# Optimization experiments

Hardware: AMD Instinct MI355X
Metric: run time of the kernel (lower is better)

## Reference

```python
import jax, jax.numpy as jnp
import numpy as np

NUM_HEADS = 12

def rel_indices(N):
    # [N, N, 3] = (dx, dy, dist^2) between patches on an img x img grid
    img = int(N ** 0.5)
    ind = jnp.arange(img)[None, :] - jnp.arange(img)[:, None]      # [img, img]
    indx = jnp.tile(ind, (img, img))                               # [N, N]
    indy = jnp.repeat(jnp.repeat(ind, img, axis=0), img, axis=1)   # [N, N]
    indd = indx ** 2 + indy ** 2
    return jnp.stack([indx, indy, indd], axis=-1).astype(jnp.float32)

def setup_inputs() -> dict:
    key = jax.random.key(0)
    ks = jax.random.split(key, 8)
    B, N, C, H = 16, 576, 768, NUM_HEADS
    std = 0.02  # trunc_normal init scale in the original
    return {
        "x": jax.random.normal(ks[0], (B, N, C), jnp.float32),
        "w_qk": jax.random.normal(ks[1], (C, 2 * C), jnp.float32) * std,
        "w_v": jax.random.normal(ks[2], (C, C), jnp.float32) * std,
        "w_proj": jax.random.normal(ks[3], (C, C), jnp.float32) * std,
        "b_proj": jnp.zeros((C,), jnp.float32),
        "w_pos": jax.random.normal(ks[4], (3, H), jnp.float32) * std,
        "b_pos": jnp.zeros((H,), jnp.float32),
        "gating": jnp.ones((H,), jnp.float32),
    }

def reference(x, w_qk, w_v, w_proj, b_proj, w_pos, b_pos, gating):
    B, N, C = x.shape
    H = NUM_HEADS
    Dh = C // H
    scale = Dh ** -0.5

    # q, k: [B, H, N, Dh]
    qk = (x @ w_qk).reshape(B, N, 2, H, Dh)
    q = jnp.transpose(qk[:, :, 0], (0, 2, 1, 3))
    k = jnp.transpose(qk[:, :, 1], (0, 2, 1, 3))

    # content scores, softmax over keys
    patch_score = jax.nn.softmax(
        jnp.einsum("bhnd,bhmd->bhnm", q, k) * scale, axis=-1)

    # positional scores: rel_indices [N,N,3] -> [H,N,N], softmax over keys
    rel = rel_indices(N)
    pos_logits = jnp.einsum("nmk,kh->hnm", rel, w_pos) + b_pos[:, None, None]
    pos_score = jax.nn.softmax(pos_logits, axis=-1)  # [H, N, N]

    # sigmoid gating + renormalization
    g = jax.nn.sigmoid(gating)[None, :, None, None]
    attn = (1.0 - g) * patch_score + g * pos_score[None]
    attn = attn / jnp.sum(attn, axis=-1, keepdims=True)

    # v: [B, H, N, Dh]
    v = jnp.transpose((x @ w_v).reshape(B, N, H, Dh), (0, 2, 1, 3))

    out = jnp.einsum("bhnm,bhmd->bnhd", attn, v).reshape(B, N, C)
    out = out @ w_proj + b_proj
    return (out, attn, v)
```

## Files before the change

kernel.cpp:

```cpp
#include <hip/hip_runtime.h>
#include <hip/hip_bf16.h>

typedef __bf16 bf16;
typedef __attribute__((ext_vector_type(4))) __bf16 bf16x4;
typedef __attribute__((ext_vector_type(8))) __bf16 bf16x8;
typedef __attribute__((ext_vector_type(4))) float floatx4;

#define BB 16
#define NN 576
#define CC 768
#define HH 12
#define DH 64

__global__ void k_convert(const float* __restrict__ in, bf16* __restrict__ out, int n4){
  int i = blockIdx.x*blockDim.x + threadIdx.x;
  if (i < n4){
    float4 f = ((const float4*)in)[i];
    bf16x4 o;
    o[0]=(bf16)f.x; o[1]=(bf16)f.y; o[2]=(bf16)f.z; o[3]=(bf16)f.w;
    ((bf16x4*)out)[i] = o;
  }
}

__global__ void k_transpose(const float* __restrict__ src, bf16* __restrict__ dst, int R, int Cc){
  __shared__ float tile[32][33];
  int c0 = blockIdx.x*32, r0 = blockIdx.y*32;
  int tx = threadIdx.x & 31, ty = threadIdx.x >> 5;
  #pragma unroll
  for (int i=0;i<4;i++)
    tile[ty + i*8][tx] = src[(size_t)(r0 + ty + i*8)*Cc + c0 + tx];
  __syncthreads();
  #pragma unroll
  for (int i=0;i<4;i++)
    dst[(size_t)(c0 + ty + i*8)*R + r0 + tx] = (bf16)tile[tx][ty + i*8];
}

__global__ __launch_bounds__(256) void k_pos(const float* __restrict__ w_pos, float* __restrict__ pos){
  int t = threadIdx.x, wv = t>>6, lane = t&63;
  int rowid = blockIdx.x*4 + wv;
  int h = rowid / NN, n = rowid % NN;
  float w0 = w_pos[h], w1 = w_pos[HH + h], w2 = w_pos[2*HH + h];
  int nx = n % 24, ny = n / 24;
  float e[9]; float mx = -1e30f;
  #pragma unroll
  for (int j=0;j<9;j++){
    int m = lane + 64*j;
    float dx = (float)(m % 24 - nx);
    float dy = (float)(m / 24 - ny);
    float l = dx*w0 + dy*w1 + (dx*dx + dy*dy)*w2;
    e[j] = l; mx = fmaxf(mx, l);
  }
  #pragma unroll
  for (int s=1;s<64;s<<=1) mx = fmaxf(mx, __shfl_xor(mx, s, 64));
  float sum = 0.f;
  #pragma unroll
  for (int j=0;j<9;j++){ e[j] = __expf(e[j]-mx); sum += e[j]; }
  #pragma unroll
  for (int s=1;s<64;s<<=1) sum += __shfl_xor(sum, s, 64);
  float inv = 1.f/sum;
  float* dst = pos + (size_t)rowid*NN;
  #pragma unroll
  for (int j=0;j<9;j++) dst[lane + 64*j] = e[j]*inv;
}

__device__ __forceinline__ void gemm_main_bf16(
    const bf16* __restrict__ A, const bf16* __restrict__ Bt,
    int lda, int ldb, int K, int rowBase, int colBase,
    bf16 (*As)[40], bf16 (*Bs)[40], floatx4* acc)
{
  int t = threadIdx.x;
  int sr = t >> 2, scg = (t & 3) * 8;
  int wv = t >> 6, m16 = t & 15, q = (t & 63) >> 4;
  for (int k0 = 0; k0 < K; k0 += 32){
    *(bf16x8*)&As[sr][scg] = *(const bf16x8*)&A[(size_t)(rowBase + sr)*lda + k0 + scg];
    *(bf16x8*)&Bs[sr][scg] = *(const bf16x8*)&Bt[(size_t)(colBase + sr)*ldb + k0 + scg];
    __syncthreads();
    bf16x8 bfr = *(const bf16x8*)&Bs[wv*16 + m16][q*8];
    #pragma unroll
    for (int rt=0; rt<4; rt++){
      bf16x8 afr = *(const bf16x8*)&As[rt*16 + m16][q*8];
      acc[rt] = __builtin_amdgcn_mfma_f32_16x16x32_bf16(afr, bfr, acc[rt], 0, 0, 0);
    }
    __syncthreads();
  }
}

__device__ __forceinline__ void gemm_main_f32A(
    const float* __restrict__ A, const bf16* __restrict__ Bt,
    int lda, int ldb, int K, int rowBase, int colBase,
    bf16 (*As)[40], bf16 (*Bs)[40], floatx4* acc)
{
  int t = threadIdx.x;
  int sr = t >> 2, scg = (t & 3) * 8;
  int wv = t >> 6, m16 = t & 15, q = (t & 63) >> 4;
  for (int k0 = 0; k0 < K; k0 += 32){
    float4 f0 = *(const float4*)&A[(size_t)(rowBase + sr)*lda + k0 + scg];
    float4 f1 = *(const float4*)&A[(size_t)(rowBase + sr)*lda + k0 + scg + 4];
    bf16x8 av;
    av[0]=(bf16)f0.x; av[1]=(bf16)f0.y; av[2]=(bf16)f0.z; av[3]=(bf16)f0.w;
    av[4]=(bf16)f1.x; av[5]=(bf16)f1.y; av[6]=(bf16)f1.z; av[7]=(bf16)f1.w;
    *(bf16x8*)&As[sr][scg] = av;
    *(bf16x8*)&Bs[sr][scg] = *(const bf16x8*)&Bt[(size_t)(colBase + sr)*ldb + k0 + scg];
    __syncthreads();
    bf16x8 bfr = *(const bf16x8*)&Bs[wv*16 + m16][q*8];
    #pragma unroll
    for (int rt=0; rt<4; rt++){
      bf16x8 afr = *(const bf16x8*)&As[rt*16 + m16][q*8];
      acc[rt] = __builtin_amdgcn_mfma_f32_16x16x32_bf16(afr, bfr, acc[rt], 0, 0, 0);
    }
    __syncthreads();
  }
}

__global__ __launch_bounds__(256) void k_gemm1(
    const bf16* __restrict__ x_bf, const bf16* __restrict__ wcatT,
    bf16* __restrict__ q_bf, bf16* __restrict__ k_bf,
    bf16* __restrict__ vt_bf, float* __restrict__ v_out)
{
  __shared__ bf16 As[64][40];
  __shared__ bf16 Bs[64][40];
  int cb = blockIdx.x % 36, rb = blockIdx.x / 36;
  int rowBase = rb*64, colBase = cb*64;
  floatx4 acc[4] = {{0.f,0.f,0.f,0.f},{0.f,0.f,0.f,0.f},{0.f,0.f,0.f,0.f},{0.f,0.f,0.f,0.f}};
  gemm_main_bf16(x_bf, wcatT, CC, CC, CC, rowBase, colBase, As, Bs, acc);
  int wv = threadIdx.x >> 6, m16 = threadIdx.x & 15, q = (threadIdx.x & 63) >> 4;
  int col = colBase + wv*16 + m16;
  #pragma unroll
  for (int rt=0; rt<4; rt++){
    #pragma unroll
    for (int i=0;i<4;i++){
      int row = rowBase + rt*16 + q*4 + i;
      float val = acc[rt][i];
      int b = row / NN, n = row % NN;
      if (col < 2*CC){
        int s = col / CC, rem = col % CC;
        int h = rem >> 6, d = rem & 63;
        bf16* dst = s ? k_bf : q_bf;
        dst[(((b*HH + h)*NN + n) << 6) + d] = (bf16)val;
      } else {
        int rem = col - 2*CC;
        int h = rem >> 6, d = rem & 63;
        v_out[(((b*HH + h)*NN + n) << 6) + d] = val;
        vt_bf[((b*HH + h)*DH + d)*NN + n] = (bf16)val;
      }
    }
  }
}

__global__ __launch_bounds__(256) void k_attn(
    const bf16* __restrict__ q_bf, const bf16* __restrict__ k_bf,
    const float* __restrict__ pos, const float* __restrict__ gating,
    float* __restrict__ attn_out)
{
  __shared__ bf16 Qs[16][72];
  __shared__ bf16 Ks[64][72];
  __shared__ float S[16][592];
  int qt = blockIdx.x % 36, bh = blockIdx.x / 36;
  int h = bh % HH;
  int n0 = qt*16;
  int t = threadIdx.x;
  int wv = t>>6, m16 = t&15, q = (t&63)>>4;
  const bf16* Qg = q_bf + ((size_t)bh*NN + n0)*DH;
  const bf16* Kg = k_bf + (size_t)bh*NN*DH;
  { int r = t >> 4, c4 = (t & 15)*4;
    *(bf16x4*)&Qs[r][c4] = *(const bf16x4*)&Qg[r*DH + c4]; }
  for (int kt=0; kt<9; kt++){
    __syncthreads();
    { int r = t>>2, cg = (t&3)*16;
      *(bf16x8*)&Ks[r][cg]   = *(const bf16x8*)&Kg[(kt*64 + r)*DH + cg];
      *(bf16x8*)&Ks[r][cg+8] = *(const bf16x8*)&Kg[(kt*64 + r)*DH + cg + 8]; }
    __syncthreads();
    floatx4 acc = {0.f,0.f,0.f,0.f};
    #pragma unroll
    for (int ks=0; ks<2; ks++){
      bf16x8 afr = *(const bf16x8*)&Qs[m16][ks*32 + q*8];
      bf16x8 bfr = *(const bf16x8*)&Ks[wv*16 + m16][ks*32 + q*8];
      acc = __builtin_amdgcn_mfma_f32_16x16x32_bf16(afr, bfr, acc, 0, 0, 0);
    }
    #pragma unroll
    for (int i=0;i<4;i++)
      S[q*4 + i][kt*64 + wv*16 + m16] = acc[i] * 0.125f;
  }
  __syncthreads();
  int row = t >> 4, sub = t & 15;
  int n = n0 + row;
  float vals[36];
  float mx = -1e30f;
  #pragma unroll
  for (int j=0;j<36;j++){ float xv = S[row][sub + 16*j]; vals[j]=xv; mx = fmaxf(mx,xv); }
  #pragma unroll
  for (int s=1;s<16;s<<=1) mx = fmaxf(mx, __shfl_xor(mx, s, 64));
  float ps = 0.f;
  #pragma unroll
  for (int j=0;j<36;j++){ vals[j] = __expf(vals[j]-mx); ps += vals[j]; }
  #pragma unroll
  for (int s=1;s<16;s<<=1) ps += __shfl_xor(ps, s, 64);
  float g = 1.f/(1.f + __expf(-gating[h]));
  float ig = (1.f - g)/ps;
  const float* posrow = pos + ((size_t)h*NN + n)*NN;
  float bs = 0.f;
  #pragma unroll
  for (int j=0;j<36;j++){ float a = ig*vals[j] + g*posrow[sub + 16*j]; vals[j]=a; bs += a; }
  #pragma unroll
  for (int s=1;s<16;s<<=1) bs += __shfl_xor(bs, s, 64);
  float inv = 1.f/bs;
  float* arow = attn_out + ((size_t)bh*NN + n)*NN;
  #pragma unroll
  for (int j=0;j<36;j++) arow[sub + 16*j] = vals[j]*inv;
}

__global__ __launch_bounds__(256) void k_pv(
    const float* __restrict__ attn, const bf16* __restrict__ vt_bf,
    bf16* __restrict__ out1_bf)
{
  __shared__ bf16 As[64][40];
  __shared__ bf16 Bs[64][40];
  int rb = blockIdx.x % 9, bh = blockIdx.x / 9;
  int b = bh / HH, h = bh % HH;
  const float* Ap = attn + (size_t)bh*NN*NN;
  const bf16* Bp = vt_bf + (size_t)bh*DH*NN;
  floatx4 acc[4] = {{0.f,0.f,0.f,0.f},{0.f,0.f,0.f,0.f},{0.f,0.f,0.f,0.f},{0.f,0.f,0.f,0.f}};
  gemm_main_f32A(Ap, Bp, NN, NN, NN, rb*64, 0, As, Bs, acc);
  int wv = threadIdx.x >> 6, m16 = threadIdx.x & 15, q = (threadIdx.x & 63) >> 4;
  int d = wv*16 + m16;
  #pragma unroll
  for (int rt=0; rt<4; rt++){
    #pragma unroll
    for (int i=0;i<4;i++){
      int n = rb*64 + rt*16 + q*4 + i;
      out1_bf[(size_t)(b*NN + n)*CC + h*DH + d] = (bf16)acc[rt][i];
    }
  }
}

__global__ __launch_bounds__(256) void k_proj(
    const bf16* __restrict__ out1_bf, const bf16* __restrict__ wprojT,
    const float* __restrict__ b_proj, float* __restrict__ out)
{
  __shared__ bf16 As[64][40];
  __shared__ bf16 Bs[64][40];
  int cb = blockIdx.x % 12, rb = blockIdx.x / 12;
  floatx4 acc[4] = {{0.f,0.f,0.f,0.f},{0.f,0.f,0.f,0.f},{0.f,0.f,0.f,0.f},{0.f,0.f,0.f,0.f}};
  gemm_main_bf16(out1_bf, wprojT, CC, CC, CC, rb*64, cb*64, As, Bs, acc);
  int wv = threadIdx.x >> 6, m16 = threadIdx.x & 15, q = (threadIdx.x & 63) >> 4;
  int col = cb*64 + wv*16 + m16;
  float bias = b_proj[col];
  #pragma unroll
  for (int rt=0; rt<4; rt++){
    #pragma unroll
    for (int i=0;i<4;i++){
      int row = rb*64 + rt*16 + q*4 + i;
      out[(size_t)row*CC + col] = acc[rt][i] + bias;
    }
  }
}

extern "C" void kernel_launch(void* const* d_in, const int* in_sizes, int n_in,
                              void* d_out, int out_size, void* d_ws, size_t ws_size,
                              hipStream_t stream)
{
  (void)in_sizes; (void)n_in; (void)out_size; (void)ws_size;
  const float* x      = (const float*)d_in[0];
  const float* w_qk   = (const float*)d_in[1];
  const float* w_v    = (const float*)d_in[2];
  const float* w_proj = (const float*)d_in[3];
  const float* b_proj = (const float*)d_in[4];
  const float* w_pos  = (const float*)d_in[5];
  const float* gating = (const float*)d_in[7];

  float* out_ptr  = (float*)d_out;
  float* attn_ptr = out_ptr + (size_t)BB*NN*CC;
  float* v_ptr    = attn_ptr + (size_t)BB*HH*NN*NN;

  char* w = (char*)d_ws;
  bf16* x_bf    = (bf16*)(w);
  bf16* wcatT   = (bf16*)(w + 14155776);
  bf16* wprojT  = (bf16*)(w + 17694720);
  bf16* q_bf    = (bf16*)(w + 18874368);
  bf16* k_bf    = (bf16*)(w + 33030144);
  bf16* vt_bf   = (bf16*)(w + 47185920);
  float* pos    = (float*)(w + 61341696);
  bf16* out1_bf = x_bf;

  k_convert<<<6912, 256, 0, stream>>>(x, x_bf, (BB*NN*CC)/4);
  k_transpose<<<dim3(48,24), 256, 0, stream>>>(w_qk, wcatT, CC, 2*CC);
  k_transpose<<<dim3(24,24), 256, 0, stream>>>(w_v, wcatT + (size_t)2*CC*CC, CC, CC);
  k_transpose<<<dim3(24,24), 256, 0, stream>>>(w_proj, wprojT, CC, CC);
  k_pos<<<(HH*NN)/4, 256, 0, stream>>>(w_pos, pos);
  k_gemm1<<<144*36, 256, 0, stream>>>(x_bf, wcatT, q_bf, k_bf, vt_bf, v_ptr);
  k_attn<<<192*36, 256, 0, stream>>>(q_bf, k_bf, pos, gating, attn_ptr);
  k_pv<<<192*9, 256, 0, stream>>>(attn_ptr, vt_bf, out1_bf);
  k_proj<<<144*12, 256, 0, stream>>>(out1_bf, wprojT, b_proj, out_ptr);
}
```

Before: 593.5 us.

## Fuse PV into attention kernel and use 128x128 LDS-direct GEMM tiles

Fuses the P@V product into the attention kernel. Normalized probabilities are written as bf16 into the reused score buffer in shared memory and multiplied against V^T there, so the 127MB fp32 attention matrix is no longer re-read from global memory. The QKV and projection GEMMs move to 128x128 tiles with four waves each computing 64x64 through 16 MFMAs per k-step. Their tiles are loaded with global_load_lds direct-to-LDS transfers. This raises per-block register use and needs the swizzled LDS layout to be consistent, while the fused kernel adds a barrier and an extra shared-memory pass.

```diff
diff --git a/kernel.cpp b/kernel.cpp
--- a/kernel.cpp
+++ b/kernel.cpp
@@ -11,6 +11,10 @@
 #define CC 768
 #define HH 12
 #define DH 64
+
+#define GLOAD_LDS16(gp, lp) __builtin_amdgcn_global_load_lds( \
+    (const __attribute__((address_space(1))) unsigned int*)(const void*)(gp), \
+    (__attribute__((address_space(3))) unsigned int*)(void*)(lp), 16, 0, 0)
 
 __global__ void k_convert(const float* __restrict__ in, bf16* __restrict__ out, int n4){
   int i = blockIdx.x*blockDim.x + threadIdx.x;
@@ -63,51 +67,32 @@
   for (int j=0;j<9;j++) dst[lane + 64*j] = e[j]*inv;
 }
 
-__device__ __forceinline__ void gemm_main_bf16(
-    const bf16* __restrict__ A, const bf16* __restrict__ Bt,
-    int lda, int ldb, int K, int rowBase, int colBase,
-    bf16 (*As)[40], bf16 (*Bs)[40], floatx4* acc)
-{
-  int t = threadIdx.x;
-  int sr = t >> 2, scg = (t & 3) * 8;
-  int wv = t >> 6, m16 = t & 15, q = (t & 63) >> 4;
+__device__ __forceinline__ void gemm128_main(
+    const bf16* __restrict__ A, const bf16* __restrict__ B,
+    int lda, int ldb, int K, bf16* As, bf16* Bs, floatx4 (*acc)[4])
+{
+  int t = threadIdx.x;
+  int w = t>>6, m16 = t&15, q = (t&63)>>4;
+  int wr = (w>>1)*64, wc = (w&1)*64;
+  int sr = t>>2, kg = (t&3)*8;
+  bf16* ldsA = As + w*512;
+  bf16* ldsB = Bs + w*512;
   for (int k0 = 0; k0 < K; k0 += 32){
-    *(bf16x8*)&As[sr][scg] = *(const bf16x8*)&A[(size_t)(rowBase + sr)*lda + k0 + scg];
-    *(bf16x8*)&Bs[sr][scg] = *(const bf16x8*)&Bt[(size_t)(colBase + sr)*ldb + k0 + scg];
-    __syncthreads();
-    bf16x8 bfr = *(const bf16x8*)&Bs[wv*16 + m16][q*8];
-    #pragma unroll
-    for (int rt=0; rt<4; rt++){
-      bf16x8 afr = *(const bf16x8*)&As[rt*16 + m16][q*8];
-      acc[rt] = __builtin_amdgcn_mfma_f32_16x16x32_bf16(afr, bfr, acc[rt], 0, 0, 0);
-    }
-    __syncthreads();
-  }
-}
-
-__device__ __forceinline__ void gemm_main_f32A(
-    const float* __restrict__ A, const bf16* __restrict__ Bt,
-    int lda, int ldb, int K, int rowBase, int colBase,
-    bf16 (*As)[40], bf16 (*Bs)[40], floatx4* acc)
-{
-  int t = threadIdx.x;
-  int sr = t >> 2, scg = (t & 3) * 8;
-  int wv = t >> 6, m16 = t & 15, q = (t & 63) >> 4;
-  for (int k0 = 0; k0 < K; k0 += 32){
-    float4 f0 = *(const float4*)&A[(size_t)(rowBase + sr)*lda + k0 + scg];
-    float4 f1 = *(const float4*)&A[(size_t)(rowBase + sr)*lda + k0 + scg + 4];
-    bf16x8 av;
-    av[0]=(bf16)f0.x; av[1]=(bf16)f0.y; av[2]=(bf16)f0.z; av[3]=(bf16)f0.w;
-    av[4]=(bf16)f1.x; av[5]=(bf16)f1.y; av[6]=(bf16)f1.z; av[7]=(bf16)f1.w;
-    *(bf16x8*)&As[sr][scg] = av;
-    *(bf16x8*)&Bs[sr][scg] = *(const bf16x8*)&Bt[(size_t)(colBase + sr)*ldb + k0 + scg];
-    __syncthreads();
-    bf16x8 bfr = *(const bf16x8*)&Bs[wv*16 + m16][q*8];
-    #pragma unroll
-    for (int rt=0; rt<4; rt++){
-      bf16x8 afr = *(const bf16x8*)&As[rt*16 + m16][q*8];
-      acc[rt] = __builtin_amdgcn_mfma_f32_16x16x32_bf16(afr, bfr, acc[rt], 0, 0, 0);
-    }
+    GLOAD_LDS16(A + (size_t)sr*lda      + k0 + kg, ldsA);
+    GLOAD_LDS16(A + (size_t)(sr+64)*lda + k0 + kg, ldsA + 2048);
+    GLOAD_LDS16(B + (size_t)sr*ldb      + k0 + kg, ldsB);
+    GLOAD_LDS16(B + (size_t)(sr+64)*ldb + k0 + kg, ldsB + 2048);
+    __syncthreads();
+    bf16x8 af[4], bfv[4];
+    #pragma unroll
+    for (int rt=0;rt<4;rt++) af[rt]  = *(const bf16x8*)&As[(wr + rt*16 + m16)*32 + q*8];
+    #pragma unroll
+    for (int ct=0;ct<4;ct++) bfv[ct] = *(const bf16x8*)&Bs[(wc + ct*16 + m16)*32 + q*8];
+    #pragma unroll
+    for (int rt=0;rt<4;rt++)
+      #pragma unroll
+      for (int ct=0;ct<4;ct++)
+        acc[rt][ct] = __builtin_amdgcn_mfma_f32_16x16x32_bf16(af[rt], bfv[ct], acc[rt][ct], 0, 0, 0);
     __syncthreads();
   }
 }
@@ -117,46 +102,57 @@
     bf16* __restrict__ q_bf, bf16* __restrict__ k_bf,
     bf16* __restrict__ vt_bf, float* __restrict__ v_out)
 {
-  __shared__ bf16 As[64][40];
-  __shared__ bf16 Bs[64][40];
-  int cb = blockIdx.x % 36, rb = blockIdx.x / 36;
-  int rowBase = rb*64, colBase = cb*64;
-  floatx4 acc[4] = {{0.f,0.f,0.f,0.f},{0.f,0.f,0.f,0.f},{0.f,0.f,0.f,0.f},{0.f,0.f,0.f,0.f}};
-  gemm_main_bf16(x_bf, wcatT, CC, CC, CC, rowBase, colBase, As, Bs, acc);
-  int wv = threadIdx.x >> 6, m16 = threadIdx.x & 15, q = (threadIdx.x & 63) >> 4;
-  int col = colBase + wv*16 + m16;
-  #pragma unroll
-  for (int rt=0; rt<4; rt++){
+  __shared__ bf16 As[128*32];
+  __shared__ bf16 Bs[128*32];
+  int cb = blockIdx.x % 18, rb = blockIdx.x / 18;
+  int rowBase = rb*128, colBase = cb*128;
+  floatx4 zero = {0.f,0.f,0.f,0.f};
+  floatx4 acc[4][4];
+  #pragma unroll
+  for (int a=0;a<4;a++)
+    #pragma unroll
+    for (int b=0;b<4;b++) acc[a][b] = zero;
+  gemm128_main(x_bf + (size_t)rowBase*CC, wcatT + (size_t)colBase*CC, CC, CC, CC, As, Bs, acc);
+  int t = threadIdx.x;
+  int w = t>>6, m16 = t&15, q = (t&63)>>4;
+  int wr = (w>>1)*64, wc = (w&1)*64;
+  #pragma unroll
+  for (int rt=0;rt<4;rt++){
     #pragma unroll
     for (int i=0;i<4;i++){
-      int row = rowBase + rt*16 + q*4 + i;
-      float val = acc[rt][i];
+      int row = rowBase + wr + rt*16 + q*4 + i;
       int b = row / NN, n = row % NN;
-      if (col < 2*CC){
-        int s = col / CC, rem = col % CC;
-        int h = rem >> 6, d = rem & 63;
-        bf16* dst = s ? k_bf : q_bf;
-        dst[(((b*HH + h)*NN + n) << 6) + d] = (bf16)val;
-      } else {
-        int rem = col - 2*CC;
-        int h = rem >> 6, d = rem & 63;
-        v_out[(((b*HH + h)*NN + n) << 6) + d] = val;
-        vt_bf[((b*HH + h)*DH + d)*NN + n] = (bf16)val;
+      #pragma unroll
+      for (int ct=0;ct<4;ct++){
+        int col = colBase + wc + ct*16 + m16;
+        float val = acc[rt][ct][i];
+        if (col < 2*CC){
+          int s = col / CC, rem = col % CC;
+          int h = rem >> 6, d = rem & 63;
+          bf16* dst = s ? k_bf : q_bf;
+          dst[(((size_t)(b*HH + h)*NN + n) << 6) + d] = (bf16)val;
+        } else {
+          int rem = col - 2*CC;
+          int h = rem >> 6, d = rem & 63;
+          v_out[(((size_t)(b*HH + h)*NN + n) << 6) + d] = val;
+          vt_bf[((size_t)(b*HH + h)*DH + d)*NN + n] = (bf16)val;
+        }
       }
     }
   }
 }
 
-__global__ __launch_bounds__(256) void k_attn(
+__global__ __launch_bounds__(256) void k_attn_pv(
     const bf16* __restrict__ q_bf, const bf16* __restrict__ k_bf,
+    const bf16* __restrict__ vt_bf,
     const float* __restrict__ pos, const float* __restrict__ gating,
-    float* __restrict__ attn_out)
+    float* __restrict__ attn_out, bf16* __restrict__ out1_bf)
 {
   __shared__ bf16 Qs[16][72];
   __shared__ bf16 Ks[64][72];
   __shared__ float S[16][592];
   int qt = blockIdx.x % 36, bh = blockIdx.x / 36;
-  int h = bh % HH;
+  int b = bh / HH, h = bh % HH;
   int n0 = qt*16;
   int t = threadIdx.x;
   int wv = t>>6, m16 = t&15, q = (t&63)>>4;
@@ -204,53 +200,59 @@
   #pragma unroll
   for (int s=1;s<16;s<<=1) bs += __shfl_xor(bs, s, 64);
   float inv = 1.f/bs;
+  __syncthreads();
   float* arow = attn_out + ((size_t)bh*NN + n)*NN;
-  #pragma unroll
-  for (int j=0;j<36;j++) arow[sub + 16*j] = vals[j]*inv;
-}
-
-__global__ __launch_bounds__(256) void k_pv(
-    const float* __restrict__ attn, const bf16* __restrict__ vt_bf,
-    bf16* __restrict__ out1_bf)
-{
-  __shared__ bf16 As[64][40];
-  __shared__ bf16 Bs[64][40];
-  int rb = blockIdx.x % 9, bh = blockIdx.x / 9;
-  int b = bh / HH, h = bh % HH;
-  const float* Ap = attn + (size_t)bh*NN*NN;
-  const bf16* Bp = vt_bf + (size_t)bh*DH*NN;
-  floatx4 acc[4] = {{0.f,0.f,0.f,0.f},{0.f,0.f,0.f,0.f},{0.f,0.f,0.f,0.f},{0.f,0.f,0.f,0.f}};
-  gemm_main_f32A(Ap, Bp, NN, NN, NN, rb*64, 0, As, Bs, acc);
-  int wv = threadIdx.x >> 6, m16 = threadIdx.x & 15, q = (threadIdx.x & 63) >> 4;
-  int d = wv*16 + m16;
-  #pragma unroll
-  for (int rt=0; rt<4; rt++){
-    #pragma unroll
-    for (int i=0;i<4;i++){
-      int n = rb*64 + rt*16 + q*4 + i;
-      out1_bf[(size_t)(b*NN + n)*CC + h*DH + d] = (bf16)acc[rt][i];
-    }
-  }
+  char* prow = (char*)(&S[0][0]) + row*2368 + ((row&3)<<4);
+  #pragma unroll
+  for (int j=0;j<36;j++){
+    float a = vals[j]*inv;
+    arow[sub + 16*j] = a;
+    *(bf16*)(prow + 2*(sub + 16*j)) = (bf16)a;
+  }
+  __syncthreads();
+  floatx4 pacc = {0.f,0.f,0.f,0.f};
+  const bf16* vrow = vt_bf + ((size_t)bh*DH + wv*16 + m16)*NN;
+  const char* pbase = (const char*)(&S[0][0]) + m16*2368 + ((m16&3)<<4) + q*16;
+  #pragma unroll
+  for (int c=0;c<18;c++){
+    bf16x8 afr = *(const bf16x8*)(pbase + c*64);
+    bf16x8 bfr = *(const bf16x8*)&vrow[c*32 + q*8];
+    pacc = __builtin_amdgcn_mfma_f32_16x16x32_bf16(afr, bfr, pacc, 0, 0, 0);
+  }
+  bf16* obase = out1_bf + ((size_t)(b*NN + n0))*CC + h*DH + wv*16 + m16;
+  #pragma unroll
+  for (int i=0;i<4;i++)
+    obase[(size_t)(q*4 + i)*CC] = (bf16)pacc[i];
 }
 
 __global__ __launch_bounds__(256) void k_proj(
     const bf16* __restrict__ out1_bf, const bf16* __restrict__ wprojT,
     const float* __restrict__ b_proj, float* __restrict__ out)
 {
-  __shared__ bf16 As[64][40];
-  __shared__ bf16 Bs[64][40];
-  int cb = blockIdx.x % 12, rb = blockIdx.x / 12;
-  floatx4 acc[4] = {{0.f,0.f,0.f,0.f},{0.f,0.f,0.f,0.f},{0.f,0.f,0.f,0.f},{0.f,0.f,0.f,0.f}};
-  gemm_main_bf16(out1_bf, wprojT, CC, CC, CC, rb*64, cb*64, As, Bs, acc);
-  int wv = threadIdx.x >> 6, m16 = threadIdx.x & 15, q = (threadIdx.x & 63) >> 4;
-  int col = cb*64 + wv*16 + m16;
-  float bias = b_proj[col];
-  #pragma unroll
-  for (int rt=0; rt<4; rt++){
+  __shared__ bf16 As[128*32];
+  __shared__ bf16 Bs[128*32];
+  int cb = blockIdx.x % 6, rb = blockIdx.x / 6;
+  int rowBase = rb*128, colBase = cb*128;
+  floatx4 zero = {0.f,0.f,0.f,0.f};
+  floatx4 acc[4][4];
+  #pragma unroll
+  for (int a=0;a<4;a++)
+    #pragma unroll
+    for (int b=0;b<4;b++) acc[a][b] = zero;
+  gemm128_main(out1_bf + (size_t)rowBase*CC, wprojT + (size_t)colBase*CC, CC, CC, CC, As, Bs, acc);
+  int t = threadIdx.x;
+  int w = t>>6, m16 = t&15, q = (t&63)>>4;
+  int wr = (w>>1)*64, wc = (w&1)*64;
+  #pragma unroll
+  for (int rt=0;rt<4;rt++){
     #pragma unroll
     for (int i=0;i<4;i++){
-      int row = rb*64 + rt*16 + q*4 + i;
-      out[(size_t)row*CC + col] = acc[rt][i] + bias;
+      int row = rowBase + wr + rt*16 + q*4 + i;
+      #pragma unroll
+      for (int ct=0;ct<4;ct++){
+        int col = colBase + wc + ct*16 + m16;
+        out[(size_t)row*CC + col] = acc[rt][ct][i] + b_proj[col];
+      }
     }
   }
 }
@@ -287,8 +289,7 @@
   k_transpose<<<dim3(24,24), 256, 0, stream>>>(w_v, wcatT + (size_t)2*CC*CC, CC, CC);
   k_transpose<<<dim3(24,24), 256, 0, stream>>>(w_proj, wprojT, CC, CC);
   k_pos<<<(HH*NN)/4, 256, 0, stream>>>(w_pos, pos);
-  k_gemm1<<<144*36, 256, 0, stream>>>(x_bf, wcatT, q_bf, k_bf, vt_bf, v_ptr);
-  k_attn<<<192*36, 256, 0, stream>>>(q_bf, k_bf, pos, gating, attn_ptr);
-  k_pv<<<192*9, 256, 0, stream>>>(attn_ptr, vt_bf, out1_bf);
-  k_proj<<<144*12, 256, 0, stream>>>(out1_bf, wprojT, b_proj, out_ptr);
-}
+  k_gemm1<<<72*18, 256, 0, stream>>>(x_bf, wcatT, q_bf, k_bf, vt_bf, v_ptr);
+  k_attn_pv<<<192*36, 256, 0, stream>>>(q_bf, k_bf, vt_bf, pos, gating, attn_ptr, out1_bf);
+  k_proj<<<72*6, 256, 0, stream>>>(out1_bf, wprojT, b_proj, out_ptr);
+}
```

New measurement: 557.9 us. 1.06x faster.
